# Performance work log

Measured on AMD Instinct MI355X. Metric: run time of the kernel, lower is better.

The kernel has to match this reference:

```python
import jax, jax.numpy as jnp
import numpy as np

T = 512        # seq_len
D = 128        # output_dim / trajectory feature dim
H_ENC = 512    # encoder hidden
H_DEC = 512    # decoder hidden
EMB = 256      # embedding size


def _lstm_step(h, c, x, Wi, Wh, bh):
    # flax LSTMCell: input dense has no bias, hidden dense has bias
    z = x @ Wi + h @ Wh + bh              # [4H]
    i, f, g, o = jnp.split(z, 4)
    i = jax.nn.sigmoid(i)
    f = jax.nn.sigmoid(f)
    g = jnp.tanh(g)
    o = jax.nn.sigmoid(o)
    c_new = f * c + i * g
    h_new = o * jnp.tanh(c_new)
    return h_new, c_new


def setup_inputs() -> dict:
    key = jax.random.key(0)
    ks = jax.random.split(key, 12)
    def w(k, shape, fan_in):
        return jax.random.normal(k, shape, dtype=jnp.float32) / np.sqrt(fan_in)
    return {
        "trajectory": jax.random.normal(ks[0], (T, D), dtype=jnp.float32),
        # encoder LSTM
        "enc_Wi": w(ks[1], (D, 4 * H_ENC), D),
        "enc_Wh": w(ks[2], (H_ENC, 4 * H_ENC), H_ENC),
        "enc_bh": jnp.zeros((4 * H_ENC,), jnp.float32),
        # encoder embedding projection
        "enc_emb_W": w(ks[3], (H_ENC, EMB), H_ENC),
        "enc_emb_b": jnp.zeros((EMB,), jnp.float32),
        # decoder initial-hidden projection from embedding
        "dec_init_W": w(ks[4], (EMB, H_DEC), EMB),
        "dec_init_b": jnp.zeros((H_DEC,), jnp.float32),
        # decoder LSTM
        "dec_Wi": w(ks[5], (D, 4 * H_DEC), D),
        "dec_Wh": w(ks[6], (H_DEC, 4 * H_DEC), H_DEC),
        "dec_bh": jnp.zeros((4 * H_DEC,), jnp.float32),
        # per-timestep decoder output Dense (fresh module each loop iter in original)
        "dec_out_W": w(ks[7], (T, H_DEC, D), H_DEC),
        "dec_out_b": jnp.zeros((T, D), jnp.float32),
    }


def reference(trajectory, enc_Wi, enc_Wh, enc_bh, enc_emb_W, enc_emb_b,
              dec_init_W, dec_init_b, dec_Wi, dec_Wh, dec_bh,
              dec_out_W, dec_out_b):
    # ---- Encoder: sequential LSTM over trajectory, zero init carry ----
    def enc_step(carry, x_t):
        h, c = carry
        h, c = _lstm_step(h, c, x_t, enc_Wi, enc_Wh, enc_bh)
        return (h, c), None
    h0 = jnp.zeros((H_ENC,), trajectory.dtype)
    c0 = jnp.zeros((H_ENC,), trajectory.dtype)
    (h, _), _ = jax.lax.scan(enc_step, (h0, c0), trajectory)
    embedding = h @ enc_emb_W + enc_emb_b  # [EMB]

    # per-timestep output Dense weights ----
    def dec_step(carry, wt):
        h, c, x = carry
        Wt, bt = wt
        h, c = _lstm_step(h, c, x, dec_Wi, dec_Wh, dec_bh)
        x = h @ Wt + bt  # flax LSTMCell output y == new h
        return (h, c, x), x
    hd0 = embedding @ dec_init_W + dec_init_b   # [H_DEC]
    cd0 = jnp.zeros((H_DEC,), trajectory.dtype)
    x0 = jnp.zeros((D,), trajectory.dtype)
    _, reconstruction = jax.lax.scan(dec_step, (hd0, cd0, x0), (dec_out_W, dec_out_b))
    return (reconstruction, embedding)
```

## Files before the change

### kernel.cpp

```cpp
#include <hip/hip_runtime.h>
#include <math.h>

#define T 512
#define D 128
#define H 512
#define EMB 256
#define Z4 2048
#define NWG 16
#define SLICE 32
#define NTH 512

typedef unsigned long long u64;
typedef unsigned int u32;

__device__ float g_xp[T * Z4];
__device__ u64 g_he[2][H];
__device__ u64 g_hd[2][H];
__device__ u64 g_xq[2][NWG][D];
__device__ float g_hd0[H];

__device__ __forceinline__ u64 aload64(const u64* p) {
    return __hip_atomic_load(p, __ATOMIC_RELAXED, __HIP_MEMORY_SCOPE_AGENT);
}
__device__ __forceinline__ void astore64(u64* p, u64 v) {
    __hip_atomic_store(p, v, __ATOMIC_RELAXED, __HIP_MEMORY_SCOPE_AGENT);
}
__device__ __forceinline__ u64 pack2(u32 tag, float v) {
    return ((u64)tag << 32) | (u64)__float_as_uint(v);
}
__device__ __forceinline__ float lo_f(u64 v) { return __uint_as_float((u32)v); }
__device__ __forceinline__ u32 hi_t(u64 v) { return (u32)(v >> 32); }

__device__ __forceinline__ float fsigm(float x) {
    x = fminf(fmaxf(x, -30.f), 30.f);
    return __builtin_amdgcn_rcpf(1.f + __expf(-x));
}
__device__ __forceinline__ float ftanh(float x) {
    x = fminf(fmaxf(x, -15.f), 15.f);
    const float e = __expf(2.f * x);
    return (e - 1.f) * __builtin_amdgcn_rcpf(e + 1.f);
}

__device__ __forceinline__ void bar_lds() {
    __builtin_amdgcn_sched_barrier(0);
    asm volatile("s_waitcnt lgkmcnt(0)" ::: "memory");
    __builtin_amdgcn_sched_barrier(0);
    __builtin_amdgcn_s_barrier();
    __builtin_amdgcn_sched_barrier(0);
}

#define TT 16
__global__ __launch_bounds__(256, 1)
void k_xp(const float* __restrict__ traj, const float* __restrict__ Wi,
          const float* __restrict__ bh) {
    const int tid = threadIdx.x;
    if (blockIdx.y == 0) {
        const int fid = blockIdx.x * 256 + tid;
        if (fid < H) {
            g_he[0][fid] = 0ull; g_he[1][fid] = 0ull;
            g_hd[0][fid] = 0ull; g_hd[1][fid] = 0ull;
        }
        u64* xqf = &g_xq[0][0][0];
        xqf[fid] = 0ull; xqf[fid + 2048] = 0ull;
    }
    const int jc = blockIdx.x;
    const int t0 = blockIdx.y * TT;
    const int j  = jc * 256 + tid;

    __shared__ float tl[TT * D];
#pragma unroll
    for (int r = 0; r < (TT * D) / 256; ++r)
        tl[r * 256 + tid] = traj[t0 * D + r * 256 + tid];
    __syncthreads();

    float acc[TT];
#pragma unroll
    for (int tt = 0; tt < TT; ++tt) acc[tt] = 0.f;
    for (int i = 0; i < D; ++i) {
        const float wv = Wi[i * Z4 + j];
#pragma unroll
        for (int tt = 0; tt < TT; ++tt) acc[tt] += tl[tt * D + i] * wv;
    }
    const float bv = bh[j];
#pragma unroll
    for (int tt = 0; tt < TT; ++tt)
        g_xp[(t0 + tt) * Z4 + j] = acc[tt] + bv;
}

__global__ __launch_bounds__(NTH, 1)
void k_enc(const float* __restrict__ Wh) {
    const int w   = blockIdx.x;
    const int tid = threadIdx.x;
    const int jl  = tid & 127;
    const int p   = tid >> 7;
    const int k0  = w * SLICE;
    const int col = (jl >> 5) * H + k0 + (jl & 31);

    float wh[128];
#pragma unroll
    for (int q = 0; q < 128; ++q)
        wh[q] = Wh[(p * 128 + q) * Z4 + col];

    __shared__ float hl[2][H];
    __shared__ float zred[NTH];

    float creg = 0.f;
    float xpv = (p == 0) ? g_xp[col] : 0.f;

    for (int t = 0; t < T; ++t) {
        const int par = t & 1;
        if (t > 0) {
            const u32 want = (u32)t;
            const u64* hp = &g_he[par][tid];
            u64 v;
            do { v = aload64(hp); } while (hi_t(v) != want);
            hl[par][tid] = lo_f(v);
        } else {
            hl[par][tid] = 0.f;
        }
        const int tn = (t + 1 < T) ? t + 1 : T - 1;
        float xpn = (p == 0) ? g_xp[tn * Z4 + col] : 0.f;

        bar_lds();

        float acc = xpv;
#pragma unroll
        for (int q4 = 0; q4 < 32; ++q4) {
            const float4 hv = *reinterpret_cast<const float4*>(&hl[par][p * 128 + q4 * 4]);
            acc += hv.x * wh[q4 * 4 + 0] + hv.y * wh[q4 * 4 + 1] +
                   hv.z * wh[q4 * 4 + 2] + hv.w * wh[q4 * 4 + 3];
        }
        zred[tid] = acc;
        bar_lds();

        if (tid < 32) {
            float zi = 0.f, zf = 0.f, zg = 0.f, zo = 0.f;
#pragma unroll
            for (int p4 = 0; p4 < 4; ++p4) {
                zi += zred[p4 * 128 +   0 + tid];
                zf += zred[p4 * 128 +  32 + tid];
                zg += zred[p4 * 128 +  64 + tid];
                zo += zred[p4 * 128 +  96 + tid];
            }
            const float cn = fsigm(zf) * creg + fsigm(zi) * ftanh(zg);
            creg = cn;
            const float hn = fsigm(zo) * ftanh(cn);
            astore64(&g_he[(t + 1) & 1][k0 + tid], pack2((u32)(t + 1), hn));
        }
        xpv = xpn;
    }
}

__global__ __launch_bounds__(256, 1)
void k_emb(const float* __restrict__ embW, const float* __restrict__ embB,
           const float* __restrict__ diW, const float* __restrict__ diB,
           float* __restrict__ out) {
    const int tid = threadIdx.x;
    __shared__ float h_l[H];
    __shared__ float e_l[EMB];
#pragma unroll
    for (int r = 0; r < H / 256; ++r)
        h_l[r * 256 + tid] = lo_f(g_he[0][r * 256 + tid]);
    __syncthreads();

    float acc = embB[tid];
    for (int i = 0; i < H; ++i)
        acc += h_l[i] * embW[i * EMB + tid];
    e_l[tid] = acc;
    out[T * D + tid] = acc;
    __syncthreads();

#pragma unroll
    for (int r = 0; r < H / 256; ++r) {
        const int k = r * 256 + tid;
        float a2 = diB[k];
        for (int e = 0; e < EMB; ++e)
            a2 += e_l[e] * diW[e * H + k];
        g_hd0[k] = a2;
    }
}

__global__ __launch_bounds__(NTH, 1)
void k_dec(const float* __restrict__ Wi, const float* __restrict__ Wh,
           const float* __restrict__ bh, const float* __restrict__ Wt,
           const float* __restrict__ bt, float* __restrict__ out) {
    const int w   = blockIdx.x;
    const int tid = threadIdx.x;
    const int jl  = tid & 127;
    const int p   = tid >> 7;
    const int k0  = w * SLICE;
    const int gcol = (jl >> 5) * H + k0 + (jl & 31);
    const int d   = tid & 127;
    const int g4  = tid >> 7;
    const int l   = tid & 63;

    float wx[32], wh[128];
#pragma unroll
    for (int q = 0; q < 32; ++q)
        wx[q] = Wi[(p * 32 + q) * Z4 + gcol];
#pragma unroll
    for (int q = 0; q < 128; ++q)
        wh[q] = Wh[(p * 128 + q) * Z4 + gcol];
    float bhi = 0.f, bhf = 0.f, bhg = 0.f, bho = 0.f;
    if (tid < 128 && l < 32) {
        bhi = bh[0 * H + k0 + l];
        bhf = bh[1 * H + k0 + l];
        bhg = bh[2 * H + k0 + l];
        bho = bh[3 * H + k0 + l];
    }

    __shared__ float h_lds[H];
    __shared__ float xs_lds[D];
    __shared__ float zred[NTH];

    float creg = 0.f;

    for (int s = 0; s < T; ++s) {
        float wpre[SLICE];
        float btv = 0.f;
        if (tid < D) {
#pragma unroll
            for (int kk = 0; kk < SLICE; ++kk)
                wpre[kk] = Wt[((size_t)s * H + k0 + kk) * D + d];
            if (w == 0) btv = bt[s * D + d];
        }

        if (s > 0) {
            const u32 want = (u32)s;
            const int par  = s & 1;
            u64 vh, v0, v1, v2, v3;
            for (;;) {
                vh = aload64(&g_hd[par][tid]);
                v0 = aload64(&g_xq[par][g4 * 4 + 0][d]);
                v1 = aload64(&g_xq[par][g4 * 4 + 1][d]);
                v2 = aload64(&g_xq[par][g4 * 4 + 2][d]);
                v3 = aload64(&g_xq[par][g4 * 4 + 3][d]);
                if ((hi_t(vh) == want) & (hi_t(v0) == want) & (hi_t(v1) == want) &
                    (hi_t(v2) == want) & (hi_t(v3) == want)) break;
            }
            h_lds[tid] = lo_f(vh);
            zred[tid]  = lo_f(v0) + lo_f(v1) + lo_f(v2) + lo_f(v3);
            bar_lds();
            if (tid < D) {
                const float xv = zred[tid] + zred[128 + tid] + zred[256 + tid] + zred[384 + tid];
                xs_lds[tid] = xv;
                if (w == 0) out[(size_t)(s - 1) * D + tid] = xv;
            }
        } else {
            h_lds[tid] = g_hd0[tid];
            if (tid < D) xs_lds[tid] = 0.f;
        }
        bar_lds();

        float acc = 0.f;
#pragma unroll
        for (int q4 = 0; q4 < 8; ++q4) {
            const float4 xv = *reinterpret_cast<const float4*>(&xs_lds[p * 32 + q4 * 4]);
            acc += xv.x * wx[q4 * 4 + 0] + xv.y * wx[q4 * 4 + 1] +
                   xv.z * wx[q4 * 4 + 2] + xv.w * wx[q4 * 4 + 3];
        }
#pragma unroll
        for (int q4 = 0; q4 < 32; ++q4) {
            const float4 hv = *reinterpret_cast<const float4*>(&h_lds[p * 128 + q4 * 4]);
            acc += hv.x * wh[q4 * 4 + 0] + hv.y * wh[q4 * 4 + 1] +
                   hv.z * wh[q4 * 4 + 2] + hv.w * wh[q4 * 4 + 3];
        }
        zred[tid] = acc;
        bar_lds();

        if (tid < 128) {
            float hn = 0.f;
            if (l < 32) {
                float zi = bhi, zf = bhf, zg = bhg, zo = bho;
#pragma unroll
                for (int p4 = 0; p4 < 4; ++p4) {
                    zi += zred[p4 * 128 +   0 + l];
                    zf += zred[p4 * 128 +  32 + l];
                    zg += zred[p4 * 128 +  64 + l];
                    zo += zred[p4 * 128 +  96 + l];
                }
                const float cn = fsigm(zf) * creg + fsigm(zi) * ftanh(zg);
                creg = cn;
                hn = fsigm(zo) * ftanh(cn);
                if (tid < 32)
                    astore64(&g_hd[(s + 1) & 1][k0 + tid], pack2((u32)(s + 1), hn));
            }
            float px = btv;
#pragma unroll
            for (int kk = 0; kk < SLICE; ++kk)
                px += __shfl(hn, kk) * wpre[kk];
            astore64(&g_xq[(s + 1) & 1][w][d], pack2((u32)(s + 1), px));
        }
    }

    if (w == 0) {
        const u32 want = (u32)T;
        u64 v0, v1, v2, v3;
        for (;;) {
            v0 = aload64(&g_xq[0][g4 * 4 + 0][d]);
            v1 = aload64(&g_xq[0][g4 * 4 + 1][d]);
            v2 = aload64(&g_xq[0][g4 * 4 + 2][d]);
            v3 = aload64(&g_xq[0][g4 * 4 + 3][d]);
            if ((hi_t(v0) == want) & (hi_t(v1) == want) &
                (hi_t(v2) == want) & (hi_t(v3) == want)) break;
        }
        zred[tid] = lo_f(v0) + lo_f(v1) + lo_f(v2) + lo_f(v3);
        bar_lds();
        if (tid < D)
            out[(size_t)(T - 1) * D + tid] =
                zred[tid] + zred[128 + tid] + zred[256 + tid] + zred[384 + tid];
    }
}

extern "C" void kernel_launch(void* const* d_in, const int* in_sizes, int n_in,
                              void* d_out, int out_size, void* d_ws, size_t ws_size,
                              hipStream_t stream) {
    const float* traj  = (const float*)d_in[0];
    const float* encWi = (const float*)d_in[1];
    const float* encWh = (const float*)d_in[2];
    const float* encbh = (const float*)d_in[3];
    const float* embW  = (const float*)d_in[4];
    const float* embB  = (const float*)d_in[5];
    const float* diW   = (const float*)d_in[6];
    const float* diB   = (const float*)d_in[7];
    const float* decWi = (const float*)d_in[8];
    const float* decWh = (const float*)d_in[9];
    const float* decbh = (const float*)d_in[10];
    const float* doW   = (const float*)d_in[11];
    const float* dob   = (const float*)d_in[12];
    float* out = (float*)d_out;

    k_xp<<<dim3(8, T / TT), dim3(256), 0, stream>>>(traj, encWi, encbh);
    k_enc<<<dim3(NWG), dim3(NTH), 0, stream>>>(encWh);
    k_emb<<<dim3(1), dim3(256), 0, stream>>>(embW, embB, diW, diB, out);
    k_dec<<<dim3(NWG), dim3(NTH), 0, stream>>>(decWi, decWh, decbh, doW, dob, out);
}
```

Before: 2.611 ms.

## Move LSTM service warps off polling waves and prefetch per-step output weights into LDS

In both encoder and decoder, the gate/activation warps are moved from the first wave to the last wave, and the polling of cross-workgroup handoff slots is restructured so the service wave does not spin. In the decoder, the per-step output-projection weights are prefetched into LDS for the next step after publishing results, so the loads overlap the wait. The x-partial reduction is split across two waves with 8 loads each. The cost is an extra barrier per step and more LDS use.

After: 2.786 ms. 1.07x slower.

```diff
diff --git a/kernel.cpp b/kernel.cpp
--- a/kernel.cpp
+++ b/kernel.cpp
@@ -95,6 +95,7 @@
     const int p   = tid >> 7;
     const int k0  = w * SLICE;
     const int col = (jl >> 5) * H + k0 + (jl & 31);
+    const int l   = tid & 63;
 
     float wh[128];
 #pragma unroll
@@ -111,12 +112,24 @@
         const int par = t & 1;
         if (t > 0) {
             const u32 want = (u32)t;
-            const u64* hp = &g_he[par][tid];
-            u64 v;
-            do { v = aload64(hp); } while (hi_t(v) != want);
-            hl[par][tid] = lo_f(v);
+            if (tid < 64) {
+                const u64* hp  = &g_he[par][tid];
+                const u64* hp2 = &g_he[par][448 + tid];
+                u64 v, v2;
+                for (;;) {
+                    v = aload64(hp); v2 = aload64(hp2);
+                    if ((hi_t(v) == want) & (hi_t(v2) == want)) break;
+                }
+                hl[par][tid] = lo_f(v);
+                hl[par][448 + tid] = lo_f(v2);
+            } else if (tid < 448) {
+                const u64* hp = &g_he[par][tid];
+                u64 v;
+                do { v = aload64(hp); } while (hi_t(v) != want);
+                hl[par][tid] = lo_f(v);
+            }
         } else {
-            hl[par][tid] = 0.f;
+            hl[0][tid] = 0.f;
         }
         const int tn = (t + 1 < T) ? t + 1 : T - 1;
         float xpn = (p == 0) ? g_xp[tn * Z4 + col] : 0.f;
@@ -133,19 +146,19 @@
         zred[tid] = acc;
         bar_lds();
 
-        if (tid < 32) {
+        if (tid >= 448 && l < 32) {
             float zi = 0.f, zf = 0.f, zg = 0.f, zo = 0.f;
 #pragma unroll
             for (int p4 = 0; p4 < 4; ++p4) {
-                zi += zred[p4 * 128 +   0 + tid];
-                zf += zred[p4 * 128 +  32 + tid];
-                zg += zred[p4 * 128 +  64 + tid];
-                zo += zred[p4 * 128 +  96 + tid];
+                zi += zred[p4 * 128 +   0 + l];
+                zf += zred[p4 * 128 +  32 + l];
+                zg += zred[p4 * 128 +  64 + l];
+                zo += zred[p4 * 128 +  96 + l];
             }
             const float cn = fsigm(zf) * creg + fsigm(zi) * ftanh(zg);
             creg = cn;
             const float hn = fsigm(zo) * ftanh(cn);
-            astore64(&g_he[(t + 1) & 1][k0 + tid], pack2((u32)(t + 1), hn));
+            astore64(&g_he[(t + 1) & 1][k0 + l], pack2((u32)(t + 1), hn));
         }
         xpv = xpn;
     }
@@ -190,9 +203,9 @@
     const int p   = tid >> 7;
     const int k0  = w * SLICE;
     const int gcol = (jl >> 5) * H + k0 + (jl & 31);
-    const int d   = tid & 127;
-    const int g4  = tid >> 7;
     const int l   = tid & 63;
+    const int sd  = tid & 127;
+    const bool svc = (tid >= 384);
 
     float wx[32], wh[128];
 #pragma unroll
@@ -202,7 +215,7 @@
     for (int q = 0; q < 128; ++q)
         wh[q] = Wh[(p * 128 + q) * Z4 + gcol];
     float bhi = 0.f, bhf = 0.f, bhg = 0.f, bho = 0.f;
-    if (tid < 128 && l < 32) {
+    if (svc && l < 32) {
         bhi = bh[0 * H + k0 + l];
         bhf = bh[1 * H + k0 + l];
         bhg = bh[2 * H + k0 + l];
@@ -212,44 +225,66 @@
     __shared__ float h_lds[H];
     __shared__ float xs_lds[D];
     __shared__ float zred[NTH];
+    __shared__ float zx[256];
+    __shared__ float wl[SLICE][D];
 
     float creg = 0.f;
+    float btv  = 0.f;
+
+    if (svc) {
+#pragma unroll
+        for (int kk = 0; kk < SLICE; ++kk)
+            wl[kk][sd] = Wt[(size_t)(k0 + kk) * D + sd];
+        if (w == 0) btv = bt[sd];
+    }
 
     for (int s = 0; s < T; ++s) {
-        float wpre[SLICE];
-        float btv = 0.f;
-        if (tid < D) {
-#pragma unroll
-            for (int kk = 0; kk < SLICE; ++kk)
-                wpre[kk] = Wt[((size_t)s * H + k0 + kk) * D + d];
-            if (w == 0) btv = bt[s * D + d];
-        }
+        const int par = s & 1;
 
         if (s > 0) {
             const u32 want = (u32)s;
-            const int par  = s & 1;
-            u64 vh, v0, v1, v2, v3;
-            for (;;) {
-                vh = aload64(&g_hd[par][tid]);
-                v0 = aload64(&g_xq[par][g4 * 4 + 0][d]);
-                v1 = aload64(&g_xq[par][g4 * 4 + 1][d]);
-                v2 = aload64(&g_xq[par][g4 * 4 + 2][d]);
-                v3 = aload64(&g_xq[par][g4 * 4 + 3][d]);
-                if ((hi_t(vh) == want) & (hi_t(v0) == want) & (hi_t(v1) == want) &
-                    (hi_t(v2) == want) & (hi_t(v3) == want)) break;
-            }
-            h_lds[tid] = lo_f(vh);
-            zred[tid]  = lo_f(v0) + lo_f(v1) + lo_f(v2) + lo_f(v3);
-            bar_lds();
-            if (tid < D) {
-                const float xv = zred[tid] + zred[128 + tid] + zred[256 + tid] + zred[384 + tid];
-                xs_lds[tid] = xv;
-                if (w == 0) out[(size_t)(s - 1) * D + tid] = xv;
+            if (tid < 128) {
+                const u64* hp  = &g_hd[par][tid];
+                const u64* hp2 = &g_hd[par][384 + tid];
+                u64 v, v2;
+                for (;;) {
+                    v = aload64(hp); v2 = aload64(hp2);
+                    if ((hi_t(v) == want) & (hi_t(v2) == want)) break;
+                }
+                h_lds[tid] = lo_f(v);
+                h_lds[384 + tid] = lo_f(v2);
+            } else if (tid < 384) {
+                const int q8 = tid - 128;
+                const int d8 = q8 & 127, hf = q8 >> 7;
+                const u64* hp = &g_hd[par][tid];
+                u64 vh, x0, x1, x2, x3, x4, x5, x6, x7;
+                for (;;) {
+                    vh = aload64(hp);
+                    x0 = aload64(&g_xq[par][hf * 8 + 0][d8]);
+                    x1 = aload64(&g_xq[par][hf * 8 + 1][d8]);
+                    x2 = aload64(&g_xq[par][hf * 8 + 2][d8]);
+                    x3 = aload64(&g_xq[par][hf * 8 + 3][d8]);
+                    x4 = aload64(&g_xq[par][hf * 8 + 4][d8]);
+                    x5 = aload64(&g_xq[par][hf * 8 + 5][d8]);
+                    x6 = aload64(&g_xq[par][hf * 8 + 6][d8]);
+                    x7 = aload64(&g_xq[par][hf * 8 + 7][d8]);
+                    if ((hi_t(vh) == want) &
+                        (hi_t(x0) == want) & (hi_t(x1) == want) &
+                        (hi_t(x2) == want) & (hi_t(x3) == want) &
+                        (hi_t(x4) == want) & (hi_t(x5) == want) &
+                        (hi_t(x6) == want) & (hi_t(x7) == want)) break;
+                }
+                h_lds[tid] = lo_f(vh);
+                zx[hf * 128 + d8] = ((lo_f(x0) + lo_f(x1)) + (lo_f(x2) + lo_f(x3))) +
+                                    ((lo_f(x4) + lo_f(x5)) + (lo_f(x6) + lo_f(x7)));
             }
         } else {
             h_lds[tid] = g_hd0[tid];
-            if (tid < D) xs_lds[tid] = 0.f;
-        }
+        }
+        bar_lds();
+
+        if (tid < 128)
+            xs_lds[tid] = (s > 0) ? (zx[tid] + zx[128 + tid]) : 0.f;
         bar_lds();
 
         float acc = 0.f;
@@ -268,7 +303,7 @@
         zred[tid] = acc;
         bar_lds();
 
-        if (tid < 128) {
+        if (svc) {
             float hn = 0.f;
             if (l < 32) {
                 float zi = bhi, zf = bhf, zg = bhg, zo = bho;
@@ -282,33 +317,49 @@
                 const float cn = fsigm(zf) * creg + fsigm(zi) * ftanh(zg);
                 creg = cn;
                 hn = fsigm(zo) * ftanh(cn);
-                if (tid < 32)
-                    astore64(&g_hd[(s + 1) & 1][k0 + tid], pack2((u32)(s + 1), hn));
+                if (tid < 416)
+                    astore64(&g_hd[(s + 1) & 1][k0 + l], pack2((u32)(s + 1), hn));
             }
             float px = btv;
 #pragma unroll
             for (int kk = 0; kk < SLICE; ++kk)
-                px += __shfl(hn, kk) * wpre[kk];
-            astore64(&g_xq[(s + 1) & 1][w][d], pack2((u32)(s + 1), px));
+                px += __shfl(hn, kk) * wl[kk][sd];
+            astore64(&g_xq[(s + 1) & 1][w][sd], pack2((u32)(s + 1), px));
+            if (w == 0 && s > 0)
+                out[(size_t)(s - 1) * D + sd] = xs_lds[sd];
+            const int sn = (s + 1 < T) ? s + 1 : T - 1;
+#pragma unroll
+            for (int kk = 0; kk < SLICE; ++kk)
+                wl[kk][sd] = Wt[((size_t)sn * H + k0 + kk) * D + sd];
+            if (w == 0) btv = bt[sn * D + sd];
         }
     }
 
     if (w == 0) {
-        const u32 want = (u32)T;
-        u64 v0, v1, v2, v3;
-        for (;;) {
-            v0 = aload64(&g_xq[0][g4 * 4 + 0][d]);
-            v1 = aload64(&g_xq[0][g4 * 4 + 1][d]);
-            v2 = aload64(&g_xq[0][g4 * 4 + 2][d]);
-            v3 = aload64(&g_xq[0][g4 * 4 + 3][d]);
-            if ((hi_t(v0) == want) & (hi_t(v1) == want) &
-                (hi_t(v2) == want) & (hi_t(v3) == want)) break;
-        }
-        zred[tid] = lo_f(v0) + lo_f(v1) + lo_f(v2) + lo_f(v3);
-        bar_lds();
-        if (tid < D)
-            out[(size_t)(T - 1) * D + tid] =
-                zred[tid] + zred[128 + tid] + zred[256 + tid] + zred[384 + tid];
+        if (tid < 256) {
+            const int d8 = tid & 127, hf = tid >> 7;
+            const u32 want = (u32)T;
+            u64 x0, x1, x2, x3, x4, x5, x6, x7;
+            for (;;) {
+                x0 = aload64(&g_xq[0][hf * 8 + 0][d8]);
+                x1 = aload64(&g_xq[0][hf * 8 + 1][d8]);
+                x2 = aload64(&g_xq[0][hf * 8 + 2][d8]);
+                x3 = aload64(&g_xq[0][hf * 8 + 3][d8]);
+                x4 = aload64(&g_xq[0][hf * 8 + 4][d8]);
+                x5 = aload64(&g_xq[0][hf * 8 + 5][d8]);
+                x6 = aload64(&g_xq[0][hf * 8 + 6][d8]);
+                x7 = aload64(&g_xq[0][hf * 8 + 7][d8]);
+                if ((hi_t(x0) == want) & (hi_t(x1) == want) &
+                    (hi_t(x2) == want) & (hi_t(x3) == want) &
+                    (hi_t(x4) == want) & (hi_t(x5) == want) &
+                    (hi_t(x6) == want) & (hi_t(x7) == want)) break;
+            }
+            zx[hf * 128 + d8] = ((lo_f(x0) + lo_f(x1)) + (lo_f(x2) + lo_f(x3))) +
+                                ((lo_f(x4) + lo_f(x5)) + (lo_f(x6) + lo_f(x7)));
+        }
+        bar_lds();
+        if (tid < 128)
+            out[(size_t)(T - 1) * D + tid] = zx[tid] + zx[128 + tid];
     }
 }
 
```
